# Kernel tuning notes

Hardware: AMD Instinct MI355X
Metric: run time of the kernel (lower is better)

## Reference

```python
import jax, jax.numpy as jnp
import numpy as np

N, C, D = 8192, 1000, 128


def setup_inputs() -> dict:
    key = jax.random.key(0)
    kx, kp = jax.random.split(key)
    x = jax.random.normal(kx, (N, D), dtype=jnp.float32)
    # Matches torch.randn(1, features_dim) per class, concatenated -> (C, D)
    prototypes = jax.random.normal(kp, (C, D), dtype=jnp.float32)
    return {"x": x, "prototypes": prototypes}


def reference(x, prototypes):
    # x: (N, D), prototypes: (C, D)
    # Faithful to: d = sum((x[:,None,:] - P[None,:,:])**2, axis=2); logits = -d
    diff = x[:, None, :] - prototypes[None, :, :]  # (N, C, D), fused by XLA
    d = jnp.sum(diff * diff, axis=2)               # (N, C)
    return -d
```

## Files before the change

### kernel.cpp

```cpp
#include <hip/hip_runtime.h>
#include <hip/hip_bf16.h>

typedef __attribute__((ext_vector_type(8))) short short8_t;
typedef __attribute__((ext_vector_type(4))) float f32x4;

static __device__ __forceinline__ unsigned short f2bf(float f) {
    unsigned int u = __float_as_uint(f);
    unsigned int r = u + 0x7fffu + ((u >> 16) & 1u);
    return (unsigned short)(r >> 16);
}

__global__ __launch_bounds__(256) void prep_kernel(
        const float* __restrict__ src, unsigned short* __restrict__ dst,
        float* __restrict__ sq, int rows_valid, int rows_total) {
    int t = threadIdx.x;
    int row = blockIdx.x * 8 + (t >> 5);
    int lane32 = t & 31;
    if (row >= rows_total) return;
    float4 v = make_float4(0.f, 0.f, 0.f, 0.f);
    if (row < rows_valid)
        v = reinterpret_cast<const float4*>(src + (size_t)row * 128)[lane32];
    ushort4 b;
    b.x = f2bf(v.x); b.y = f2bf(v.y); b.z = f2bf(v.z); b.w = f2bf(v.w);
    reinterpret_cast<ushort4*>(dst + (size_t)row * 128)[lane32] = b;
    float s = v.x*v.x + v.y*v.y + v.z*v.z + v.w*v.w;
    #pragma unroll
    for (int m = 16; m >= 1; m >>= 1) s += __shfl_xor(s, m, 64);
    if (lane32 == 0) sq[row] = s;
}

#define BM 128
#define BN 64
#define LDA 136

__global__ __launch_bounds__(256) void gemm_kernel(
        const unsigned short* __restrict__ A,
        const unsigned short* __restrict__ B,
        const float* __restrict__ xsq, const float* __restrict__ psq,
        float* __restrict__ out) {
    __shared__ unsigned short As[BM][LDA];
    __shared__ unsigned short Bs[BN][LDA];
    __shared__ float xq_s[BM];
    __shared__ float pq_s[BN];

    int t = threadIdx.x;
    int bm = blockIdx.x & 63;
    int bn = blockIdx.x >> 6;
    const int rowA0 = bm * BM;
    const int rowB0 = bn * BN;

    #pragma unroll
    for (int it = 0; it < 8; ++it) {
        int idx = it * 256 + t;
        int r = idx >> 4;
        int c = (idx & 15) * 8;
        short8_t v = *reinterpret_cast<const short8_t*>(A + (size_t)(rowA0 + r) * 128 + c);
        *reinterpret_cast<short8_t*>(&As[r][c]) = v;
    }
    #pragma unroll
    for (int it = 0; it < 4; ++it) {
        int idx = it * 256 + t;
        int r = idx >> 4;
        int c = (idx & 15) * 8;
        short8_t v = *reinterpret_cast<const short8_t*>(B + (size_t)(rowB0 + r) * 128 + c);
        *reinterpret_cast<short8_t*>(&Bs[r][c]) = v;
    }
    if (t < BM) xq_s[t] = xsq[rowA0 + t];
    if (t < BN) pq_s[t] = psq[rowB0 + t];
    __syncthreads();

    int wave = t >> 6;
    int lane = t & 63;
    int wm = (wave >> 1) * 64;
    int wn = (wave & 1) * 32;
    int lr = lane & 15;
    int lk = (lane >> 4) * 8;

    f32x4 acc[4][2] = {};
    #pragma unroll
    for (int ks = 0; ks < 4; ++ks) {
        int k0 = ks * 32 + lk;
        short8_t a[4], b[2];
        #pragma unroll
        for (int mi = 0; mi < 4; ++mi)
            a[mi] = *reinterpret_cast<const short8_t*>(&As[wm + mi * 16 + lr][k0]);
        #pragma unroll
        for (int ni = 0; ni < 2; ++ni)
            b[ni] = *reinterpret_cast<const short8_t*>(&Bs[wn + ni * 16 + lr][k0]);
        #pragma unroll
        for (int mi = 0; mi < 4; ++mi)
            #pragma unroll
            for (int ni = 0; ni < 2; ++ni)
                acc[mi][ni] = __builtin_amdgcn_mfma_f32_16x16x32_bf16(
                        a[mi], b[ni], acc[mi][ni], 0, 0, 0);
    }

    int mrow_base = (lane >> 4) * 4;
    #pragma unroll
    for (int mi = 0; mi < 4; ++mi) {
        #pragma unroll
        for (int ni = 0; ni < 2; ++ni) {
            int cl = wn + ni * 16 + lr;
            int c = rowB0 + cl;
            if (c < 1000) {
                float pq = pq_s[cl];
                #pragma unroll
                for (int j = 0; j < 4; ++j) {
                    int ml = wm + mi * 16 + mrow_base + j;
                    int m = rowA0 + ml;
                    out[(size_t)m * 1000 + c] = 2.f * acc[mi][ni][j] - xq_s[ml] - pq;
                }
            }
        }
    }
}

__global__ __launch_bounds__(256) void naive_kernel(
        const float* __restrict__ x, const float* __restrict__ p,
        float* __restrict__ out) {
    long long idx = (long long)blockIdx.x * 256 + threadIdx.x;
    if (idx >= (long long)8192 * 1000) return;
    int n = (int)(idx / 1000);
    int c = (int)(idx % 1000);
    const float4* xr = reinterpret_cast<const float4*>(x + (size_t)n * 128);
    const float4* pr = reinterpret_cast<const float4*>(p + (size_t)c * 128);
    float d = 0.f;
    #pragma unroll
    for (int i = 0; i < 32; ++i) {
        float4 a = xr[i], b = pr[i];
        float dx = a.x - b.x, dy = a.y - b.y, dz = a.z - b.z, dw = a.w - b.w;
        d += dx * dx + dy * dy + dz * dz + dw * dw;
    }
    out[idx] = -d;
}

extern "C" void kernel_launch(void* const* d_in, const int* in_sizes, int n_in,
                              void* d_out, int out_size, void* d_ws, size_t ws_size,
                              hipStream_t stream) {
    const float* x = (const float*)d_in[0];
    const float* p = (const float*)d_in[1];
    float* out = (float*)d_out;

    const size_t xb_elems = (size_t)8192 * 128;
    const size_t pb_elems = (size_t)1024 * 128;
    const size_t need = xb_elems * 2 + pb_elems * 2 + 8192 * 4 + 1024 * 4;

    if (ws_size >= need) {
        unsigned short* xb = (unsigned short*)d_ws;
        unsigned short* pb = xb + xb_elems;
        float* xsq = (float*)(pb + pb_elems);
        float* psq = xsq + 8192;
        prep_kernel<<<1024, 256, 0, stream>>>(x, xb, xsq, 8192, 8192);
        prep_kernel<<<128, 256, 0, stream>>>(p, pb, psq, 1000, 1024);
        gemm_kernel<<<1024, 256, 0, stream>>>(xb, pb, xsq, psq, out);
    } else {
        naive_kernel<<<((size_t)8192 * 1000 + 255) / 256, 256, 0, stream>>>(x, p, out);
    }
}
```

Measured before the change: 23.01 us.

## Fuse bf16 conversion and squared-norm prep into the distance GEMM kernel

Removes the two prep launches and their workspace round-trip. The GEMM kernel now loads fp32 x and prototypes directly, converts them to bf16 while staging into shared memory, and computes the row squared norms with a 16-lane shuffle reduction. It also swaps the block mapping so consecutive blocks share the same x tile and walk across the prototype tiles, which helps L2 reuse of the larger input. The cost is that each block reloads and reconverts fp32 data that other blocks also convert, doubling global read bytes per tile, and the naive fallback path is dropped.

New measurement: 23.67 us. 2.9% more time.

```diff
diff --git a/kernel.cpp b/kernel.cpp
--- a/kernel.cpp
+++ b/kernel.cpp
@@ -10,33 +10,13 @@
     return (unsigned short)(r >> 16);
 }
 
-__global__ __launch_bounds__(256) void prep_kernel(
-        const float* __restrict__ src, unsigned short* __restrict__ dst,
-        float* __restrict__ sq, int rows_valid, int rows_total) {
-    int t = threadIdx.x;
-    int row = blockIdx.x * 8 + (t >> 5);
-    int lane32 = t & 31;
-    if (row >= rows_total) return;
-    float4 v = make_float4(0.f, 0.f, 0.f, 0.f);
-    if (row < rows_valid)
-        v = reinterpret_cast<const float4*>(src + (size_t)row * 128)[lane32];
-    ushort4 b;
-    b.x = f2bf(v.x); b.y = f2bf(v.y); b.z = f2bf(v.z); b.w = f2bf(v.w);
-    reinterpret_cast<ushort4*>(dst + (size_t)row * 128)[lane32] = b;
-    float s = v.x*v.x + v.y*v.y + v.z*v.z + v.w*v.w;
-    #pragma unroll
-    for (int m = 16; m >= 1; m >>= 1) s += __shfl_xor(s, m, 64);
-    if (lane32 == 0) sq[row] = s;
-}
-
 #define BM 128
 #define BN 64
 #define LDA 136
 
-__global__ __launch_bounds__(256) void gemm_kernel(
-        const unsigned short* __restrict__ A,
-        const unsigned short* __restrict__ B,
-        const float* __restrict__ xsq, const float* __restrict__ psq,
+__global__ __launch_bounds__(256) void fused_kernel(
+        const float* __restrict__ X,
+        const float* __restrict__ P,
         float* __restrict__ out) {
     __shared__ unsigned short As[BM][LDA];
     __shared__ unsigned short Bs[BN][LDA];
@@ -44,8 +24,8 @@
     __shared__ float pq_s[BN];
 
     int t = threadIdx.x;
-    int bm = blockIdx.x & 63;
-    int bn = blockIdx.x >> 6;
+    int bn = blockIdx.x & 15;
+    int bm = blockIdx.x >> 4;
     const int rowA0 = bm * BM;
     const int rowB0 = bn * BN;
 
@@ -53,20 +33,49 @@
     for (int it = 0; it < 8; ++it) {
         int idx = it * 256 + t;
         int r = idx >> 4;
-        int c = (idx & 15) * 8;
-        short8_t v = *reinterpret_cast<const short8_t*>(A + (size_t)(rowA0 + r) * 128 + c);
-        *reinterpret_cast<short8_t*>(&As[r][c]) = v;
+        int c8 = (idx & 15) * 8;
+        const float4* src = reinterpret_cast<const float4*>(X + (size_t)(rowA0 + r) * 128 + c8);
+        float4 v0 = src[0], v1 = src[1];
+        short8_t b;
+        b[0] = (short)f2bf(v0.x); b[1] = (short)f2bf(v0.y);
+        b[2] = (short)f2bf(v0.z); b[3] = (short)f2bf(v0.w);
+        b[4] = (short)f2bf(v1.x); b[5] = (short)f2bf(v1.y);
+        b[6] = (short)f2bf(v1.z); b[7] = (short)f2bf(v1.w);
+        *reinterpret_cast<short8_t*>(&As[r][c8]) = b;
+        float s = v0.x*v0.x + v0.y*v0.y + v0.z*v0.z + v0.w*v0.w
+                + v1.x*v1.x + v1.y*v1.y + v1.z*v1.z + v1.w*v1.w;
+        s += __shfl_xor(s, 1, 64);
+        s += __shfl_xor(s, 2, 64);
+        s += __shfl_xor(s, 4, 64);
+        s += __shfl_xor(s, 8, 64);
+        if ((t & 15) == 0) xq_s[r] = s;
     }
     #pragma unroll
     for (int it = 0; it < 4; ++it) {
         int idx = it * 256 + t;
         int r = idx >> 4;
-        int c = (idx & 15) * 8;
-        short8_t v = *reinterpret_cast<const short8_t*>(B + (size_t)(rowB0 + r) * 128 + c);
-        *reinterpret_cast<short8_t*>(&Bs[r][c]) = v;
+        int c8 = (idx & 15) * 8;
+        int gr = rowB0 + r;
+        float4 v0 = make_float4(0.f, 0.f, 0.f, 0.f);
+        float4 v1 = make_float4(0.f, 0.f, 0.f, 0.f);
+        if (gr < 1000) {
+            const float4* src = reinterpret_cast<const float4*>(P + (size_t)gr * 128 + c8);
+            v0 = src[0]; v1 = src[1];
+        }
+        short8_t b;
+        b[0] = (short)f2bf(v0.x); b[1] = (short)f2bf(v0.y);
+        b[2] = (short)f2bf(v0.z); b[3] = (short)f2bf(v0.w);
+        b[4] = (short)f2bf(v1.x); b[5] = (short)f2bf(v1.y);
+        b[6] = (short)f2bf(v1.z); b[7] = (short)f2bf(v1.w);
+        *reinterpret_cast<short8_t*>(&Bs[r][c8]) = b;
+        float s = v0.x*v0.x + v0.y*v0.y + v0.z*v0.z + v0.w*v0.w
+                + v1.x*v1.x + v1.y*v1.y + v1.z*v1.z + v1.w*v1.w;
+        s += __shfl_xor(s, 1, 64);
+        s += __shfl_xor(s, 2, 64);
+        s += __shfl_xor(s, 4, 64);
+        s += __shfl_xor(s, 8, 64);
+        if ((t & 15) == 0) pq_s[r] = s;
     }
-    if (t < BM) xq_s[t] = xsq[rowA0 + t];
-    if (t < BN) pq_s[t] = psq[rowB0 + t];
     __syncthreads();
 
     int wave = t >> 6;
@@ -115,45 +124,12 @@
     }
 }
 
-__global__ __launch_bounds__(256) void naive_kernel(
-        const float* __restrict__ x, const float* __restrict__ p,
-        float* __restrict__ out) {
-    long long idx = (long long)blockIdx.x * 256 + threadIdx.x;
-    if (idx >= (long long)8192 * 1000) return;
-    int n = (int)(idx / 1000);
-    int c = (int)(idx % 1000);
-    const float4* xr = reinterpret_cast<const float4*>(x + (size_t)n * 128);
-    const float4* pr = reinterpret_cast<const float4*>(p + (size_t)c * 128);
-    float d = 0.f;
-    #pragma unroll
-    for (int i = 0; i < 32; ++i) {
-        float4 a = xr[i], b = pr[i];
-        float dx = a.x - b.x, dy = a.y - b.y, dz = a.z - b.z, dw = a.w - b.w;
-        d += dx * dx + dy * dy + dz * dz + dw * dw;
-    }
-    out[idx] = -d;
-}
-
 extern "C" void kernel_launch(void* const* d_in, const int* in_sizes, int n_in,
                               void* d_out, int out_size, void* d_ws, size_t ws_size,
                               hipStream_t stream) {
     const float* x = (const float*)d_in[0];
     const float* p = (const float*)d_in[1];
     float* out = (float*)d_out;
-
-    const size_t xb_elems = (size_t)8192 * 128;
-    const size_t pb_elems = (size_t)1024 * 128;
-    const size_t need = xb_elems * 2 + pb_elems * 2 + 8192 * 4 + 1024 * 4;
-
-    if (ws_size >= need) {
-        unsigned short* xb = (unsigned short*)d_ws;
-        unsigned short* pb = xb + xb_elems;
-        float* xsq = (float*)(pb + pb_elems);
-        float* psq = xsq + 8192;
-        prep_kernel<<<1024, 256, 0, stream>>>(x, xb, xsq, 8192, 8192);
-        prep_kernel<<<128, 256, 0, stream>>>(p, pb, psq, 1000, 1024);
-        gemm_kernel<<<1024, 256, 0, stream>>>(xb, pb, xsq, psq, out);
-    } else {
-        naive_kernel<<<((size_t)8192 * 1000 + 255) / 256, 256, 0, stream>>>(x, p, out);
-    }
+    (void)d_ws; (void)ws_size;
+    fused_kernel<<<1024, 256, 0, stream>>>(x, p, out);
 }
```

## Fuse x conversion into GEMM, loop over prototype tiles with double-buffered LDS

Applied to the files above, without the earlier changes.

Removes the separate x prep kernel: each block converts a 32-row slab of x to bf16 and computes its squared norms in-kernel. The block then loops over all prototypes in 128-column chunks, double-buffering the B tiles in LDS with register prefetch. Output is transposed through LDS so each lane writes float4 rows. This cuts a kernel launch and the workspace round trip for x, and widens stores. It runs only 256 blocks with a serial 8-step loop, so there is less parallelism per block.

Result: slower. 24.43 us (+6.2%).

```diff
diff --git a/kernel.cpp b/kernel.cpp
--- a/kernel.cpp
+++ b/kernel.cpp
@@ -29,88 +29,109 @@
     if (lane32 == 0) sq[row] = s;
 }
 
-#define BM 128
-#define BN 64
-#define LDA 136
+#define LDT 136
 
-__global__ __launch_bounds__(256) void gemm_kernel(
-        const unsigned short* __restrict__ A,
-        const unsigned short* __restrict__ B,
-        const float* __restrict__ xsq, const float* __restrict__ psq,
+__global__ __launch_bounds__(512) void main_kernel(
+        const float* __restrict__ X,
+        const unsigned short* __restrict__ Bw,
+        const float* __restrict__ psq,
         float* __restrict__ out) {
-    __shared__ unsigned short As[BM][LDA];
-    __shared__ unsigned short Bs[BN][LDA];
-    __shared__ float xq_s[BM];
-    __shared__ float pq_s[BN];
+    __shared__ unsigned short As[32][LDT];
+    __shared__ unsigned short Bs[2][128][LDT];
+    __shared__ float xq_s[32];
+    __shared__ float trans[8][16][16];
 
-    int t = threadIdx.x;
-    int bm = blockIdx.x & 63;
-    int bn = blockIdx.x >> 6;
-    const int rowA0 = bm * BM;
-    const int rowB0 = bn * BN;
+    const int t = threadIdx.x;
+    const int slab0 = blockIdx.x * 32;
 
-    #pragma unroll
-    for (int it = 0; it < 8; ++it) {
-        int idx = it * 256 + t;
-        int r = idx >> 4;
-        int c = (idx & 15) * 8;
-        short8_t v = *reinterpret_cast<const short8_t*>(A + (size_t)(rowA0 + r) * 128 + c);
-        *reinterpret_cast<short8_t*>(&As[r][c]) = v;
+    {
+        int r = t >> 4;
+        int c8 = (t & 15) * 8;
+        const float4* src = reinterpret_cast<const float4*>(X + (size_t)(slab0 + r) * 128 + c8);
+        float4 v0 = src[0], v1 = src[1];
+        short8_t b;
+        b[0] = (short)f2bf(v0.x); b[1] = (short)f2bf(v0.y);
+        b[2] = (short)f2bf(v0.z); b[3] = (short)f2bf(v0.w);
+        b[4] = (short)f2bf(v1.x); b[5] = (short)f2bf(v1.y);
+        b[6] = (short)f2bf(v1.z); b[7] = (short)f2bf(v1.w);
+        *reinterpret_cast<short8_t*>(&As[r][c8]) = b;
+        float s = v0.x*v0.x + v0.y*v0.y + v0.z*v0.z + v0.w*v0.w
+                + v1.x*v1.x + v1.y*v1.y + v1.z*v1.z + v1.w*v1.w;
+        s += __shfl_xor(s, 1, 64);
+        s += __shfl_xor(s, 2, 64);
+        s += __shfl_xor(s, 4, 64);
+        s += __shfl_xor(s, 8, 64);
+        if ((t & 15) == 0) xq_s[r] = s;
     }
-    #pragma unroll
-    for (int it = 0; it < 4; ++it) {
-        int idx = it * 256 + t;
-        int r = idx >> 4;
-        int c = (idx & 15) * 8;
-        short8_t v = *reinterpret_cast<const short8_t*>(B + (size_t)(rowB0 + r) * 128 + c);
-        *reinterpret_cast<short8_t*>(&Bs[r][c]) = v;
+    {
+        int r = t >> 2;
+        int cb = (t & 3) * 32;
+        const unsigned short* src = Bw + (size_t)r * 128 + cb;
+        #pragma unroll
+        for (int k = 0; k < 4; ++k) {
+            short8_t v = *reinterpret_cast<const short8_t*>(src + k * 8);
+            *reinterpret_cast<short8_t*>(&Bs[0][r][cb + k * 8]) = v;
+        }
     }
-    if (t < BM) xq_s[t] = xsq[rowA0 + t];
-    if (t < BN) pq_s[t] = psq[rowB0 + t];
     __syncthreads();
 
-    int wave = t >> 6;
-    int lane = t & 63;
-    int wm = (wave >> 1) * 64;
-    int wn = (wave & 1) * 32;
-    int lr = lane & 15;
-    int lk = (lane >> 4) * 8;
+    const int wave = t >> 6;
+    const int lane = t & 63;
+    const int wm  = (wave >> 2) * 16;
+    const int wcb = (wave & 3) * 32;
+    const int lr  = lane & 15;
+    const int lkb = (lane >> 4) * 8;
 
-    f32x4 acc[4][2] = {};
+    short8_t afrag[4];
     #pragma unroll
-    for (int ks = 0; ks < 4; ++ks) {
-        int k0 = ks * 32 + lk;
-        short8_t a[4], b[2];
-        #pragma unroll
-        for (int mi = 0; mi < 4; ++mi)
-            a[mi] = *reinterpret_cast<const short8_t*>(&As[wm + mi * 16 + lr][k0]);
-        #pragma unroll
-        for (int ni = 0; ni < 2; ++ni)
-            b[ni] = *reinterpret_cast<const short8_t*>(&Bs[wn + ni * 16 + lr][k0]);
-        #pragma unroll
-        for (int mi = 0; mi < 4; ++mi)
+    for (int ks = 0; ks < 4; ++ks)
+        afrag[ks] = *reinterpret_cast<const short8_t*>(&As[wm + lr][ks * 32 + lkb]);
+    const float4 xq4 = *reinterpret_cast<const float4*>(&xq_s[wm + (lane >> 4) * 4]);
+
+    const int rr = lane >> 2;
+    const int cq = (lane & 3) * 4;
+    const int rbase = (lane >> 4) * 4;
+
+    int cur = 0;
+    #pragma unroll 1
+    for (int cn = 0; cn < 8; ++cn) {
+        short8_t pf[4];
+        if (cn < 7) {
+            int r = t >> 2;
+            int cb = (t & 3) * 32;
+            const unsigned short* src = Bw + (size_t)((cn + 1) * 128 + r) * 128 + cb;
             #pragma unroll
-            for (int ni = 0; ni < 2; ++ni)
-                acc[mi][ni] = __builtin_amdgcn_mfma_f32_16x16x32_bf16(
-                        a[mi], b[ni], acc[mi][ni], 0, 0, 0);
-    }
-
-    int mrow_base = (lane >> 4) * 4;
-    #pragma unroll
-    for (int mi = 0; mi < 4; ++mi) {
+            for (int k = 0; k < 4; ++k)
+                pf[k] = *reinterpret_cast<const short8_t*>(src + k * 8);
+        }
         #pragma unroll
         for (int ni = 0; ni < 2; ++ni) {
-            int cl = wn + ni * 16 + lr;
-            int c = rowB0 + cl;
-            if (c < 1000) {
-                float pq = pq_s[cl];
-                #pragma unroll
-                for (int j = 0; j < 4; ++j) {
-                    int ml = wm + mi * 16 + mrow_base + j;
-                    int m = rowA0 + ml;
-                    out[(size_t)m * 1000 + c] = 2.f * acc[mi][ni][j] - xq_s[ml] - pq;
-                }
+            f32x4 acc = {0.f, 0.f, 0.f, 0.f};
+            #pragma unroll
+            for (int ks = 0; ks < 4; ++ks) {
+                short8_t bfrag = *reinterpret_cast<const short8_t*>(
+                        &Bs[cur][wcb + ni * 16 + lr][ks * 32 + lkb]);
+                acc = __builtin_amdgcn_mfma_f32_16x16x32_bf16(afrag[ks], bfrag, acc, 0, 0, 0);
             }
+            #pragma unroll
+            for (int j = 0; j < 4; ++j)
+                trans[wave][rbase + j][lr] = 2.f * acc[j] - ((const float*)&xq4)[j];
+            float4 tv = *reinterpret_cast<const float4*>(&trans[wave][rr][cq]);
+            int col = cn * 128 + wcb + ni * 16 + cq;
+            if (col < 1000) {
+                float4 pq = *reinterpret_cast<const float4*>(psq + col);
+                tv.x -= pq.x; tv.y -= pq.y; tv.z -= pq.z; tv.w -= pq.w;
+                *reinterpret_cast<float4*>(out + (size_t)(slab0 + wm + rr) * 1000 + col) = tv;
+            }
+        }
+        if (cn < 7) {
+            int r = t >> 2;
+            int cb = (t & 3) * 32;
+            #pragma unroll
+            for (int k = 0; k < 4; ++k)
+                *reinterpret_cast<short8_t*>(&Bs[cur ^ 1][r][cb + k * 8]) = pf[k];
+            __syncthreads();
+            cur ^= 1;
         }
     }
 }
@@ -141,18 +162,14 @@
     const float* p = (const float*)d_in[1];
     float* out = (float*)d_out;
 
-    const size_t xb_elems = (size_t)8192 * 128;
     const size_t pb_elems = (size_t)1024 * 128;
-    const size_t need = xb_elems * 2 + pb_elems * 2 + 8192 * 4 + 1024 * 4;
+    const size_t need = pb_elems * 2 + 1024 * 4;
 
     if (ws_size >= need) {
-        unsigned short* xb = (unsigned short*)d_ws;
-        unsigned short* pb = xb + xb_elems;
-        float* xsq = (float*)(pb + pb_elems);
-        float* psq = xsq + 8192;
-        prep_kernel<<<1024, 256, 0, stream>>>(x, xb, xsq, 8192, 8192);
+        unsigned short* pb = (unsigned short*)d_ws;
+        float* psq = (float*)(pb + pb_elems);
         prep_kernel<<<128, 256, 0, stream>>>(p, pb, psq, 1000, 1024);
-        gemm_kernel<<<1024, 256, 0, stream>>>(xb, pb, xsq, psq, out);
+        main_kernel<<<256, 512, 0, stream>>>(x, pb, psq, out);
     } else {
         naive_kernel<<<((size_t)8192 * 1000 + 255) / 256, 256, 0, stream>>>(x, p, out);
     }
```

## Retile GEMM to 64x128 with XCD-aware block mapping and nontemporal stores

Applied to the files above, without the earlier changes.

Switches the block tile from 128 rows of x by 64 prototypes to 64 rows by 128 prototypes, so each wave now computes a 32x64 subtile. Block indices are remapped so consecutive workgroups, which are spread across the XCDs, share the same x tile inside an XCD's L2. Output writes become nontemporal stores so the large result does not pollute the cache. The wider prototype tile leaves more padded columns (1024 vs 1000) inside one block, and the load pattern changes to fewer, wider per-thread loads.

After: 30.50 us. 32.6% more time.

```diff
diff --git a/kernel.cpp b/kernel.cpp
--- a/kernel.cpp
+++ b/kernel.cpp
@@ -29,86 +29,89 @@
     if (lane32 == 0) sq[row] = s;
 }
 
-#define BM 128
-#define BN 64
 #define LDA 136
 
 __global__ __launch_bounds__(256) void gemm_kernel(
-        const unsigned short* __restrict__ A,
-        const unsigned short* __restrict__ B,
-        const float* __restrict__ xsq, const float* __restrict__ psq,
+        const unsigned short* __restrict__ Xb,
+        const unsigned short* __restrict__ Pb,
+        const float* __restrict__ xsq,
+        const float* __restrict__ psq,
         float* __restrict__ out) {
-    __shared__ unsigned short As[BM][LDA];
-    __shared__ unsigned short Bs[BN][LDA];
-    __shared__ float xq_s[BM];
-    __shared__ float pq_s[BN];
+    __shared__ unsigned short As[64][LDA];
+    __shared__ unsigned short Bs[128][LDA];
+    __shared__ float xq_s[64];
+    __shared__ float pq_s[128];
 
-    int t = threadIdx.x;
-    int bm = blockIdx.x & 63;
-    int bn = blockIdx.x >> 6;
-    const int rowA0 = bm * BM;
-    const int rowB0 = bn * BN;
+    const int t = threadIdx.x;
+    const int wg  = blockIdx.x;
+    const int idx = wg >> 3;
+    const int bm  = (wg & 7) * 16 + (idx >> 3);
+    const int bn  = idx & 7;
+    const int rowA0 = bm * 64;
+    const int rowB0 = bn * 128;
 
-    #pragma unroll
-    for (int it = 0; it < 8; ++it) {
-        int idx = it * 256 + t;
-        int r = idx >> 4;
-        int c = (idx & 15) * 8;
-        short8_t v = *reinterpret_cast<const short8_t*>(A + (size_t)(rowA0 + r) * 128 + c);
-        *reinterpret_cast<short8_t*>(&As[r][c]) = v;
+    {
+        int r = t >> 2, c0 = (t & 3) * 32;
+        const short8_t* src = reinterpret_cast<const short8_t*>(
+                Xb + (size_t)(rowA0 + r) * 128 + c0);
+        short8_t v0 = src[0], v1 = src[1], v2 = src[2], v3 = src[3];
+        short8_t* dst = reinterpret_cast<short8_t*>(&As[r][c0]);
+        dst[0] = v0; dst[1] = v1; dst[2] = v2; dst[3] = v3;
     }
-    #pragma unroll
-    for (int it = 0; it < 4; ++it) {
-        int idx = it * 256 + t;
-        int r = idx >> 4;
-        int c = (idx & 15) * 8;
-        short8_t v = *reinterpret_cast<const short8_t*>(B + (size_t)(rowB0 + r) * 128 + c);
-        *reinterpret_cast<short8_t*>(&Bs[r][c]) = v;
+    {
+        int r = t >> 1, c0 = (t & 1) * 64;
+        const short8_t* src = reinterpret_cast<const short8_t*>(
+                Pb + (size_t)(rowB0 + r) * 128 + c0);
+        short8_t v0 = src[0], v1 = src[1], v2 = src[2], v3 = src[3];
+        short8_t v4 = src[4], v5 = src[5], v6 = src[6], v7 = src[7];
+        short8_t* dst = reinterpret_cast<short8_t*>(&Bs[r][c0]);
+        dst[0] = v0; dst[1] = v1; dst[2] = v2; dst[3] = v3;
+        dst[4] = v4; dst[5] = v5; dst[6] = v6; dst[7] = v7;
     }
-    if (t < BM) xq_s[t] = xsq[rowA0 + t];
-    if (t < BN) pq_s[t] = psq[rowB0 + t];
+    if (t < 64)  xq_s[t] = xsq[rowA0 + t];
+    if (t < 128) pq_s[t] = psq[rowB0 + t];
     __syncthreads();
 
-    int wave = t >> 6;
-    int lane = t & 63;
-    int wm = (wave >> 1) * 64;
-    int wn = (wave & 1) * 32;
-    int lr = lane & 15;
-    int lk = (lane >> 4) * 8;
+    const int wave = t >> 6;
+    const int lane = t & 63;
+    const int wm = (wave >> 1) * 32;
+    const int wn = (wave & 1) * 64;
+    const int lr = lane & 15;
+    const int lkb = (lane >> 4) * 8;
+    const int rbase = (lane >> 4) * 4;
 
-    f32x4 acc[4][2] = {};
+    f32x4 acc[2][4] = {};
     #pragma unroll
     for (int ks = 0; ks < 4; ++ks) {
-        int k0 = ks * 32 + lk;
-        short8_t a[4], b[2];
+        int k0 = ks * 32 + lkb;
+        short8_t a[2], b[4];
         #pragma unroll
-        for (int mi = 0; mi < 4; ++mi)
+        for (int mi = 0; mi < 2; ++mi)
             a[mi] = *reinterpret_cast<const short8_t*>(&As[wm + mi * 16 + lr][k0]);
         #pragma unroll
-        for (int ni = 0; ni < 2; ++ni)
+        for (int ni = 0; ni < 4; ++ni)
             b[ni] = *reinterpret_cast<const short8_t*>(&Bs[wn + ni * 16 + lr][k0]);
         #pragma unroll
-        for (int mi = 0; mi < 4; ++mi)
+        for (int mi = 0; mi < 2; ++mi)
             #pragma unroll
-            for (int ni = 0; ni < 2; ++ni)
+            for (int ni = 0; ni < 4; ++ni)
                 acc[mi][ni] = __builtin_amdgcn_mfma_f32_16x16x32_bf16(
                         a[mi], b[ni], acc[mi][ni], 0, 0, 0);
     }
 
-    int mrow_base = (lane >> 4) * 4;
     #pragma unroll
-    for (int mi = 0; mi < 4; ++mi) {
+    for (int mi = 0; mi < 2; ++mi) {
         #pragma unroll
-        for (int ni = 0; ni < 2; ++ni) {
+        for (int ni = 0; ni < 4; ++ni) {
             int cl = wn + ni * 16 + lr;
             int c = rowB0 + cl;
             if (c < 1000) {
                 float pq = pq_s[cl];
                 #pragma unroll
                 for (int j = 0; j < 4; ++j) {
-                    int ml = wm + mi * 16 + mrow_base + j;
-                    int m = rowA0 + ml;
-                    out[(size_t)m * 1000 + c] = 2.f * acc[mi][ni][j] - xq_s[ml] - pq;
+                    int ml = wm + mi * 16 + rbase + j;
+                    float v = 2.f * acc[mi][ni][j] - xq_s[ml] - pq;
+                    __builtin_nontemporal_store(v, out + (size_t)(rowA0 + ml) * 1000 + c);
                 }
             }
         }
```
